# Optimization experiments

Measured on AMD Instinct MI355X. Metric: run time of the kernel, lower is better.

Reference implementation:

```python
import jax, jax.numpy as jnp
import numpy as np

N = 150000
E = 600000
IN_DIM = 128
HID = 64


def setup_inputs() -> dict:
    key = jax.random.key(0)
    ks = jax.random.split(key, 8)
    obs = jax.random.normal(ks[0], (N, IN_DIM), dtype=jnp.float32)
    edge_index = jax.random.randint(ks[1], (2, E), 0, N, dtype=jnp.int64)
    # GCNConv / Linear parameters (PyTorch layout: W is [out, in])
    W1 = jax.random.normal(ks[2], (HID, IN_DIM), dtype=jnp.float32) / np.sqrt(IN_DIM)
    b1 = jnp.zeros((HID,), dtype=jnp.float32)
    W2 = jax.random.normal(ks[3], (HID, HID), dtype=jnp.float32) / np.sqrt(HID)
    b2 = jnp.zeros((HID,), dtype=jnp.float32)
    W3 = jax.random.normal(ks[4], (1, HID), dtype=jnp.float32) / np.sqrt(HID)
    b3 = jnp.zeros((1,), dtype=jnp.float32)
    return {"obs": obs, "edge_index": edge_index, "W1": W1, "b1": b1,
            "W2": W2, "b2": b2, "W3": W3, "b3": b3}


def _gcn_norm(edge_index, n):
    # PyG gcn_norm: add self-loops, symmetric normalization D^-1/2 A D^-1/2
    loops = jnp.arange(n, dtype=edge_index.dtype)
    row = jnp.concatenate([edge_index[0], loops])  # source
    col = jnp.concatenate([edge_index[1], loops])  # target
    deg = jax.ops.segment_sum(jnp.ones(row.shape[0], jnp.float32), col, num_segments=n)
    dinv = jnp.where(deg > 0, jax.lax.rsqrt(deg), 0.0)
    norm = dinv[row] * dinv[col]  # [E+N]
    return row, col, norm


def _gcn_conv(x, row, col, norm, n, W, b):
    # x' = lin(x); out[col] += norm * x'[row]; out += bias
    xw = x @ W.T                     # [N, out]
    msg = xw[row] * norm[:, None]    # gather + scale, [E+N, out]
    out = jax.ops.segment_sum(msg, col, num_segments=n)
    return out + b


def reference(obs, edge_index, W1, b1, W2, b2, W3, b3):
    n = obs.shape[0]
    row, col, norm = _gcn_norm(edge_index, n)
    h1 = jax.nn.relu(_gcn_conv(obs, row, col, norm, n, W1, b1))
    h2 = jax.nn.relu(_gcn_conv(h1, row, col, norm, n, W2, b2))
    out = h2 @ W3.T + b3             # [N, 1]
    out = out.reshape(-1, 15)[:, 3:].reshape(-1)  # drop first 3 of every 15
    return out
```

## Files before the change

kernel.cpp:

```cpp
#include <hip/hip_runtime.h>

#define NN 150000
#define NE 600000
#define IND 128
#define HID 64
#define KMAX 32
#define BSHIFT 9
#define NBUCK 293
#define SUBCAP 384
#define PARTB 586
#define CVTB 32
#define GEMM_GRID ((NN + 63) / 64)
#define NOUT 120000

typedef short s16x8 __attribute__((ext_vector_type(8)));
typedef float f32x4 __attribute__((ext_vector_type(4)));

__device__ __forceinline__ unsigned f2bf(float f) {
    unsigned u = __float_as_uint(f);
    return (u + 0x7FFFu + ((u >> 16) & 1u)) >> 16;
}

#define ACC4(v, dr) \
    a0 = fmaf(__uint_as_float((v).x << 16), dr, a0); \
    a1 = fmaf(__uint_as_float((v).x & 0xFFFF0000u), dr, a1); \
    a2 = fmaf(__uint_as_float((v).y << 16), dr, a2); \
    a3 = fmaf(__uint_as_float((v).y & 0xFFFF0000u), dr, a3);

__global__ void k_zero(int* __restrict__ gcnt) {
    int t = blockIdx.x * 256 + threadIdx.x;
    if (t < NBUCK * 8) gcnt[t] = 0;
}

__global__ __launch_bounds__(256) void k_init(
        const int* __restrict__ rowv, const int* __restrict__ colv,
        int* __restrict__ gcnt, int2* __restrict__ ebuf,
        const float* __restrict__ W1, const float* __restrict__ W2,
        unsigned short* __restrict__ W1b, unsigned short* __restrict__ W2b) {
    int tid = threadIdx.x;
    if (blockIdx.x < PARTB) {
        __shared__ int hist[NBUCK];
        __shared__ int bases[NBUCK];
        for (int i = tid; i < NBUCK; i += 256) hist[i] = 0;
        __syncthreads();
        int t = blockIdx.x * 256 + tid;
        bool valid = (t < NE / 4);
        int4 r4, c4;
        int bk[4], sl[4];
        if (valid) {
            r4 = ((const int4*)rowv)[t];
            c4 = ((const int4*)colv)[t];
            bk[0] = c4.x >> BSHIFT; sl[0] = atomicAdd(&hist[bk[0]], 1);
            bk[1] = c4.y >> BSHIFT; sl[1] = atomicAdd(&hist[bk[1]], 1);
            bk[2] = c4.z >> BSHIFT; sl[2] = atomicAdd(&hist[bk[2]], 1);
            bk[3] = c4.w >> BSHIFT; sl[3] = atomicAdd(&hist[bk[3]], 1);
        }
        __syncthreads();
        int xcd = blockIdx.x & 7;
        for (int i = tid; i < NBUCK; i += 256)
            bases[i] = hist[i] ? atomicAdd(&gcnt[i * 8 + xcd], hist[i]) : 0;
        __syncthreads();
        if (valid) {
            #pragma unroll
            for (int e = 0; e < 4; ++e) {
                int c = (e == 0) ? c4.x : (e == 1) ? c4.y : (e == 2) ? c4.z : c4.w;
                int r = (e == 0) ? r4.x : (e == 1) ? r4.y : (e == 2) ? r4.z : r4.w;
                int p = bases[bk[e]] + sl[e];
                if (p < SUBCAP) ebuf[(bk[e] * 8 + xcd) * SUBCAP + p] = make_int2(c, r);
            }
        }
        return;
    }
    int t = (blockIdx.x - PARTB) * 256 + tid;
    if (t < HID * IND) W1b[t] = (unsigned short)f2bf(W1[t]);
    if (t < HID * HID) W2b[t] = (unsigned short)f2bf(W2[t]);
}

__global__ __launch_bounds__(256) void k_sort_gemm1(
        const float* __restrict__ obs, const unsigned short* __restrict__ W1b,
        unsigned short* __restrict__ xs,
        const int* __restrict__ gcnt, const int2* __restrict__ ebuf,
        int* __restrict__ cursor, float* __restrict__ dinvf,
        int* __restrict__ csr_src) {
    __shared__ char smem[64 * IND * 2];
    int tid = threadIdx.x;
    if (blockIdx.x < NBUCK) {
        int k = blockIdx.x;
        int lo = k << BSHIFT;
        int* cnt = (int*)smem;
        for (int i = tid; i < 512; i += 256) cnt[i] = 0;
        __syncthreads();
        for (int x = 0; x < 8; ++x) {
            int len = gcnt[k * 8 + x]; if (len > SUBCAP) len = SUBCAP;
            const int2* run = ebuf + (size_t)(k * 8 + x) * SUBCAP;
            for (int i = tid; i < len; i += 256) {
                int2 e = run[i];
                int s = atomicAdd(&cnt[e.x - lo], 1);
                if (s < KMAX) csr_src[e.x * KMAX + s] = e.y;
            }
        }
        __syncthreads();
        for (int i = tid; i < 512; i += 256) {
            int n = lo + i;
            if (n < NN) {
                cursor[n] = cnt[i];
                dinvf[n] = rsqrtf((float)(cnt[i] + 1));
            }
        }
        return;
    }
    char* sB = smem;
    int base = (blockIdx.x - NBUCK) * 64;

    {
        const uint4* Wsrc = (const uint4*)W1b;
        for (int idx = tid; idx < 8 * IND; idx += 256) {
            int row = idx >> 4, c8 = idx & 15;
            uint4 v = Wsrc[idx];
            int byte = row * (IND * 2) + c8 * 16;
            byte ^= (row & 7) << 4;
            *(uint4*)(sB + byte) = v;
        }
    }
    __syncthreads();

    int wave = tid >> 6, lane = tid & 63;
    int r16 = lane & 15, kg = lane >> 4;
    int arow = base + 16 * wave + r16;
    if (arow >= NN) arow = NN - 1;
    const float4* Ap = (const float4*)(obs + (size_t)arow * IND) + kg * 2;

    float4 va[8];
    #pragma unroll
    for (int s = 0; s < 4; ++s) {
        va[2 * s]     = Ap[s * 8];
        va[2 * s + 1] = Ap[s * 8 + 1];
    }

    f32x4 acc[4];
    #pragma unroll
    for (int j = 0; j < 4; ++j) acc[j] = (f32x4){0.f, 0.f, 0.f, 0.f};

    #pragma unroll
    for (int s = 0; s < 4; ++s) {
        float4 v0 = va[2 * s], v1 = va[2 * s + 1];
        s16x8 a;
        a[0] = (short)f2bf(v0.x); a[1] = (short)f2bf(v0.y);
        a[2] = (short)f2bf(v0.z); a[3] = (short)f2bf(v0.w);
        a[4] = (short)f2bf(v1.x); a[5] = (short)f2bf(v1.y);
        a[6] = (short)f2bf(v1.z); a[7] = (short)f2bf(v1.w);
        int kb = (s * 32 + kg * 8) * 2;
        #pragma unroll
        for (int j = 0; j < 4; ++j) {
            int row = 16 * j + r16;
            int byte = row * (IND * 2) + kb;
            byte ^= (row & 7) << 4;
            s16x8 b = *(const s16x8*)(sB + byte);
            acc[j] = __builtin_amdgcn_mfma_f32_16x16x32_bf16(a, b, acc[j], 0, 0, 0);
        }
    }

    #pragma unroll
    for (int r = 0; r < 4; ++r) {
        int n = base + 16 * wave + kg * 4 + r;
        if (n >= NN) continue;
        #pragma unroll
        for (int j = 0; j < 4; ++j) {
            int c = 16 * j + r16;
            xs[(size_t)n * HID + c] = (unsigned short)f2bf(acc[j][r]);
        }
    }
}

__global__ __launch_bounds__(256) void k_agg_gemm(
        const unsigned short* __restrict__ xs, const int* __restrict__ cursor,
        const float* __restrict__ dinvf, const int* __restrict__ csr_src,
        const float* __restrict__ bias, const unsigned short* __restrict__ W2b,
        unsigned short* __restrict__ xs2) {
    __shared__ char smem[2 * 64 * HID * 2];
    char* sA = smem;
    char* sB = smem + 64 * HID * 2;
    int tid = threadIdx.x;
    int base = blockIdx.x * 64;

    {
        const uint4* Wsrc = (const uint4*)W2b;
        for (int idx = tid; idx < 8 * HID; idx += 256) {
            int row = idx >> 3, c8 = idx & 7;
            uint4 v = Wsrc[idx];
            int byte = row * (HID * 2) + c8 * 16;
            byte ^= (row & 7) << 4;
            *(uint4*)(sB + byte) = v;
        }
    }

    int lane = tid & 63;
    int l16 = lane & 15, gbase = lane & 48;
    int grp = tid >> 4;
    const uint2* src = (const uint2*)xs;
    float4 bb = ((const float4*)bias)[l16];

    int degA[4], cntA[4], idxA[4];
    uint2 svA[4];
    float drA[4];
    #pragma unroll
    for (int s4 = 0; s4 < 4; ++s4) {
        int node = base + s4 * 16 + grp;
        bool ok = node < NN;
        int nc = ok ? node : NN - 1;
        int deg = cursor[nc];
        degA[s4] = deg;
        cntA[s4] = ok ? (deg < KMAX ? deg : KMAX) : 0;
        idxA[s4] = csr_src[nc * KMAX + l16];
        svA[s4]  = src[(size_t)nc * 16 + l16];
    }
    #pragma unroll
    for (int s4 = 0; s4 < 4; ++s4) {
        int safe = (l16 < cntA[s4]) ? idxA[s4] : 0;
        drA[s4] = dinvf[safe];
    }

    #pragma unroll
    for (int s4 = 0; s4 < 4; ++s4) {
        int row = s4 * 16 + grp;
        int node = base + row;
        int cnt = cntA[s4];
        float dn = rsqrtf((float)(degA[s4] + 1));
        uint2 sv = svA[s4];
        float a0 = __uint_as_float(sv.x << 16) * dn;
        float a1 = __uint_as_float(sv.x & 0xFFFF0000u) * dn;
        float a2 = __uint_as_float(sv.y << 16) * dn;
        float a3 = __uint_as_float(sv.y & 0xFFFF0000u) * dn;
        #pragma unroll
        for (int j = 0; j < 8; ++j) {
            int r    = __shfl(idxA[s4], gbase + j, 64);
            float dr = __shfl(drA[s4], gbase + j, 64);
            if (j < cnt) {
                uint2 v = src[(size_t)r * 16 + l16];
                ACC4(v, dr)
            }
        }
        if (cnt > 8) {
            int c16 = cnt < 16 ? cnt : 16;
            for (int j = 8; j < c16; ++j) {
                int r    = __shfl(idxA[s4], gbase + j, 64);
                float dr = __shfl(drA[s4], gbase + j, 64);
                uint2 v = src[(size_t)r * 16 + l16];
                ACC4(v, dr)
            }
            for (int j = 16; j < cnt; ++j) {
                int r = csr_src[node * KMAX + j];
                float dr = dinvf[r];
                uint2 v = src[(size_t)r * 16 + l16];
                ACC4(v, dr)
            }
        }
        float h0 = fmaxf(fmaf(dn, a0, bb.x), 0.f);
        float h1 = fmaxf(fmaf(dn, a1, bb.y), 0.f);
        float h2 = fmaxf(fmaf(dn, a2, bb.z), 0.f);
        float h3 = fmaxf(fmaf(dn, a3, bb.w), 0.f);
        uint2 o;
        o.x = f2bf(h0) | (f2bf(h1) << 16);
        o.y = f2bf(h2) | (f2bf(h3) << 16);
        if (node >= NN) { o.x = 0u; o.y = 0u; }
        int byte = row * (HID * 2) + l16 * 8;
        byte ^= (row & 7) << 4;
        *(uint2*)(sA + byte) = o;
    }
    __syncthreads();

    int wave = tid >> 6;
    int wr = wave >> 1, wc = wave & 1;
    int r16 = lane & 15, kg = lane >> 4;

    f32x4 acc[2][2];
    #pragma unroll
    for (int i = 0; i < 2; ++i)
        #pragma unroll
        for (int j = 0; j < 2; ++j)
            acc[i][j] = (f32x4){0.f, 0.f, 0.f, 0.f};

    #pragma unroll
    for (int s = 0; s < HID / 32; ++s) {
        int kb = (s * 32 + kg * 8) * 2;
        s16x8 a[2], b[2];
        #pragma unroll
        for (int i = 0; i < 2; ++i) {
            int row = 32 * wr + 16 * i + r16;
            int byte = row * (HID * 2) + kb;
            byte ^= (row & 7) << 4;
            a[i] = *(const s16x8*)(sA + byte);
        }
        #pragma unroll
        for (int j = 0; j < 2; ++j) {
            int row = 32 * wc + 16 * j + r16;
            int byte = row * (HID * 2) + kb;
            byte ^= (row & 7) << 4;
            b[j] = *(const s16x8*)(sB + byte);
        }
        #pragma unroll
        for (int i = 0; i < 2; ++i)
            #pragma unroll
            for (int j = 0; j < 2; ++j)
                acc[i][j] = __builtin_amdgcn_mfma_f32_16x16x32_bf16(a[i], b[j], acc[i][j], 0, 0, 0);
    }

    #pragma unroll
    for (int i = 0; i < 2; ++i) {
        #pragma unroll
        for (int r = 0; r < 4; ++r) {
            int n = base + 32 * wr + 16 * i + kg * 4 + r;
            if (n >= NN) continue;
            float d = dinvf[n];
            #pragma unroll
            for (int j = 0; j < 2; ++j) {
                int c = 32 * wc + 16 * j + r16;
                xs2[(size_t)n * HID + c] = (unsigned short)f2bf(acc[i][j][r] * d);
            }
        }
    }
}

__global__ __launch_bounds__(256) void k_agg_out(const unsigned short* __restrict__ xs,
                      const int* __restrict__ cursor, const int* __restrict__ csr_src,
                      const float* __restrict__ bias, const float* __restrict__ W3,
                      const float* __restrict__ b3, float* __restrict__ outp) {
    int tid = threadIdx.x;
    int lane = tid & 63;
    int l16 = lane & 15, gbase = lane & 48;
    int q = blockIdx.x * 16 + (tid >> 4);
    if (q >= NOUT) return;
    int g15 = q / 12, jj12 = q - g15 * 12;
    int node = g15 * 15 + 3 + jj12;
    int deg = cursor[node];
    int cnt = deg < KMAX ? deg : KMAX;
    float dn = rsqrtf((float)(deg + 1));
    const uint2* src = (const uint2*)xs;
    int idx0 = csr_src[node * KMAX + l16];
    uint2 sv = src[(size_t)node * 16 + l16];
    float a0 = __uint_as_float(sv.x << 16);
    float a1 = __uint_as_float(sv.x & 0xFFFF0000u);
    float a2 = __uint_as_float(sv.y << 16);
    float a3 = __uint_as_float(sv.y & 0xFFFF0000u);
    #pragma unroll
    for (int j = 0; j < 8; ++j) {
        int r = __shfl(idx0, gbase + j, 64);
        if (j < cnt) {
            uint2 v = src[(size_t)r * 16 + l16];
            ACC4(v, 1.0f)
        }
    }
    if (cnt > 8) {
        int c16 = cnt < 16 ? cnt : 16;
        for (int j = 8; j < c16; ++j) {
            int r = __shfl(idx0, gbase + j, 64);
            uint2 v = src[(size_t)r * 16 + l16];
            ACC4(v, 1.0f)
        }
        for (int j = 16; j < cnt; ++j) {
            int r = csr_src[node * KMAX + j];
            uint2 v = src[(size_t)r * 16 + l16];
            ACC4(v, 1.0f)
        }
    }
    float4 bb = ((const float4*)bias)[l16];
    float h0 = fmaxf(fmaf(dn, a0, bb.x), 0.f);
    float h1 = fmaxf(fmaf(dn, a1, bb.y), 0.f);
    float h2 = fmaxf(fmaf(dn, a2, bb.z), 0.f);
    float h3 = fmaxf(fmaf(dn, a3, bb.w), 0.f);
    float4 ww = ((const float4*)W3)[l16];
    float v = h0 * ww.x + h1 * ww.y + h2 * ww.z + h3 * ww.w;
    v += __shfl_xor(v, 1, 64);
    v += __shfl_xor(v, 2, 64);
    v += __shfl_xor(v, 4, 64);
    v += __shfl_xor(v, 8, 64);
    if (l16 == 0) outp[q] = v + b3[0];
}

extern "C" void kernel_launch(void* const* d_in, const int* in_sizes, int n_in,
                              void* d_out, int out_size, void* d_ws, size_t ws_size,
                              hipStream_t stream) {
    const float* obs = (const float*)d_in[0];
    const int*   ei  = (const int*)d_in[1];
    const float* W1  = (const float*)d_in[2];
    const float* b1  = (const float*)d_in[3];
    const float* W2  = (const float*)d_in[4];
    const float* b2  = (const float*)d_in[5];
    const float* W3  = (const float*)d_in[6];
    const float* b3  = (const float*)d_in[7];
    float* out = (float*)d_out;

    char* ws = (char*)d_ws;
    size_t off = 0;
    auto alloc = [&](size_t bytes) -> void* {
        void* p = ws + off;
        off += (bytes + 255) & ~(size_t)255;
        return p;
    };
    int*   gcnt    = (int*)  alloc((size_t)NBUCK * 8 * 4);
    int*   cursor  = (int*)  alloc((size_t)NN * 4);
    float* dinvf   = (float*)alloc((size_t)NN * 4);
    int*   csr_src = (int*)  alloc((size_t)NN * KMAX * 4);
    int2*  ebuf    = (int2*) alloc((size_t)NBUCK * 8 * SUBCAP * 8);
    unsigned short* XB  = (unsigned short*)alloc((size_t)NN * HID * 2);
    unsigned short* XB2 = (unsigned short*)alloc((size_t)NN * HID * 2);
    unsigned short* W1b = (unsigned short*)alloc((size_t)HID * IND * 2);
    unsigned short* W2b = (unsigned short*)alloc((size_t)HID * HID * 2);

    const int* rowv = ei;
    const int* colv = ei + NE;

    k_zero<<<(NBUCK * 8 + 255) / 256, 256, 0, stream>>>(gcnt);
    k_init<<<PARTB + CVTB, 256, 0, stream>>>(rowv, colv, gcnt, ebuf, W1, W2, W1b, W2b);
    k_sort_gemm1<<<NBUCK + GEMM_GRID, 256, 0, stream>>>(obs, W1b, XB, gcnt, ebuf,
                                                        cursor, dinvf, csr_src);
    k_agg_gemm<<<GEMM_GRID, 256, 0, stream>>>(XB, cursor, dinvf, csr_src, b1, W2b, XB2);
    k_agg_out<<<(NOUT + 15) / 16, 256, 0, stream>>>(XB2, cursor, csr_src, b2, W3, b3, out);
}
```

Before: 110.5 us.

## Fuse GEMM1 with edge partitioning, split sort kernel, batch gather loads

GEMM1 (obs×W1) moves into the partition kernel so it runs alongside edge bucketing, and the CSR sort becomes its own kernel with finer 256-node buckets. The weight fp32→bf16 conversion kernel is dropped; each GEMM block converts W1/W2 directly into shared memory. The aggregation loops issue all eight neighbor gathers before accumulating, using zero weights for padding lanes, to raise memory-level parallelism. The cost is redundant per-block weight conversion and extra loads of row 0 for padding lanes. Smaller bucket capacity raises the risk of overflow truncation.

```diff
diff --git a/kernel.cpp b/kernel.cpp
--- a/kernel.cpp
+++ b/kernel.cpp
@@ -5,11 +5,10 @@
 #define IND 128
 #define HID 64
 #define KMAX 32
-#define BSHIFT 9
-#define NBUCK 293
-#define SUBCAP 384
+#define BSHIFT 8
+#define NBUCK 586
+#define SUBCAP 224
 #define PARTB 586
-#define CVTB 32
 #define GEMM_GRID ((NN + 63) / 64)
 #define NOUT 120000
 
@@ -35,12 +34,13 @@
 __global__ __launch_bounds__(256) void k_init(
         const int* __restrict__ rowv, const int* __restrict__ colv,
         int* __restrict__ gcnt, int2* __restrict__ ebuf,
-        const float* __restrict__ W1, const float* __restrict__ W2,
-        unsigned short* __restrict__ W1b, unsigned short* __restrict__ W2b) {
+        const float* __restrict__ obs, const float* __restrict__ W1,
+        unsigned short* __restrict__ xs) {
+    __shared__ char smem[64 * IND * 2];
     int tid = threadIdx.x;
     if (blockIdx.x < PARTB) {
-        __shared__ int hist[NBUCK];
-        __shared__ int bases[NBUCK];
+        int* hist  = (int*)smem;
+        int* bases = hist + NBUCK;
         for (int i = tid; i < NBUCK; i += 256) hist[i] = 0;
         __syncthreads();
         int t = blockIdx.x * 256 + tid;
@@ -71,55 +71,20 @@
         }
         return;
     }
-    int t = (blockIdx.x - PARTB) * 256 + tid;
-    if (t < HID * IND) W1b[t] = (unsigned short)f2bf(W1[t]);
-    if (t < HID * HID) W2b[t] = (unsigned short)f2bf(W2[t]);
-}
-
-__global__ __launch_bounds__(256) void k_sort_gemm1(
-        const float* __restrict__ obs, const unsigned short* __restrict__ W1b,
-        unsigned short* __restrict__ xs,
-        const int* __restrict__ gcnt, const int2* __restrict__ ebuf,
-        int* __restrict__ cursor, float* __restrict__ dinvf,
-        int* __restrict__ csr_src) {
-    __shared__ char smem[64 * IND * 2];
-    int tid = threadIdx.x;
-    if (blockIdx.x < NBUCK) {
-        int k = blockIdx.x;
-        int lo = k << BSHIFT;
-        int* cnt = (int*)smem;
-        for (int i = tid; i < 512; i += 256) cnt[i] = 0;
-        __syncthreads();
-        for (int x = 0; x < 8; ++x) {
-            int len = gcnt[k * 8 + x]; if (len > SUBCAP) len = SUBCAP;
-            const int2* run = ebuf + (size_t)(k * 8 + x) * SUBCAP;
-            for (int i = tid; i < len; i += 256) {
-                int2 e = run[i];
-                int s = atomicAdd(&cnt[e.x - lo], 1);
-                if (s < KMAX) csr_src[e.x * KMAX + s] = e.y;
-            }
-        }
-        __syncthreads();
-        for (int i = tid; i < 512; i += 256) {
-            int n = lo + i;
-            if (n < NN) {
-                cursor[n] = cnt[i];
-                dinvf[n] = rsqrtf((float)(cnt[i] + 1));
-            }
-        }
-        return;
-    }
     char* sB = smem;
-    int base = (blockIdx.x - NBUCK) * 64;
+    int base = (blockIdx.x - PARTB) * 64;
 
     {
-        const uint4* Wsrc = (const uint4*)W1b;
-        for (int idx = tid; idx < 8 * IND; idx += 256) {
-            int row = idx >> 4, c8 = idx & 15;
-            uint4 v = Wsrc[idx];
-            int byte = row * (IND * 2) + c8 * 16;
+        const float4* Wsrc = (const float4*)W1;
+        for (int idx = tid; idx < 64 * 32; idx += 256) {
+            int row = idx >> 5, c4i = idx & 31;
+            float4 w = Wsrc[idx];
+            uint2 p;
+            p.x = f2bf(w.x) | (f2bf(w.y) << 16);
+            p.y = f2bf(w.z) | (f2bf(w.w) << 16);
+            int byte = row * (IND * 2) + c4i * 8;
             byte ^= (row & 7) << 4;
-            *(uint4*)(sB + byte) = v;
+            *(uint2*)(sB + byte) = p;
         }
     }
     __syncthreads();
@@ -172,10 +137,37 @@
     }
 }
 
+__global__ __launch_bounds__(256) void k_sort(
+        const int* __restrict__ gcnt, const int2* __restrict__ ebuf,
+        int* __restrict__ cursor, float* __restrict__ dinvf,
+        int* __restrict__ csr_src) {
+    __shared__ int cnt[256];
+    int tid = threadIdx.x;
+    int k = blockIdx.x;
+    int lo = k << BSHIFT;
+    cnt[tid] = 0;
+    __syncthreads();
+    for (int x = 0; x < 8; ++x) {
+        int len = gcnt[k * 8 + x]; if (len > SUBCAP) len = SUBCAP;
+        const int2* run = ebuf + (size_t)(k * 8 + x) * SUBCAP;
+        for (int i = tid; i < len; i += 256) {
+            int2 e = run[i];
+            int s = atomicAdd(&cnt[e.x - lo], 1);
+            if (s < KMAX) csr_src[e.x * KMAX + s] = e.y;
+        }
+    }
+    __syncthreads();
+    int n = lo + tid;
+    if (n < NN) {
+        cursor[n] = cnt[tid];
+        dinvf[n] = rsqrtf((float)(cnt[tid] + 1));
+    }
+}
+
 __global__ __launch_bounds__(256) void k_agg_gemm(
         const unsigned short* __restrict__ xs, const int* __restrict__ cursor,
         const float* __restrict__ dinvf, const int* __restrict__ csr_src,
-        const float* __restrict__ bias, const unsigned short* __restrict__ W2b,
+        const float* __restrict__ bias, const float* __restrict__ W2,
         unsigned short* __restrict__ xs2) {
     __shared__ char smem[2 * 64 * HID * 2];
     char* sA = smem;
@@ -184,13 +176,16 @@
     int base = blockIdx.x * 64;
 
     {
-        const uint4* Wsrc = (const uint4*)W2b;
-        for (int idx = tid; idx < 8 * HID; idx += 256) {
-            int row = idx >> 3, c8 = idx & 7;
-            uint4 v = Wsrc[idx];
-            int byte = row * (HID * 2) + c8 * 16;
+        const float4* Wsrc = (const float4*)W2;
+        for (int idx = tid; idx < 64 * 16; idx += 256) {
+            int row = idx >> 4, c4i = idx & 15;
+            float4 w = Wsrc[idx];
+            uint2 p;
+            p.x = f2bf(w.x) | (f2bf(w.y) << 16);
+            p.y = f2bf(w.z) | (f2bf(w.w) << 16);
+            int byte = row * (HID * 2) + c4i * 8;
             byte ^= (row & 7) << 4;
-            *(uint4*)(sB + byte) = v;
+            *(uint2*)(sB + byte) = p;
         }
     }
 
@@ -216,8 +211,7 @@
     }
     #pragma unroll
     for (int s4 = 0; s4 < 4; ++s4) {
-        int safe = (l16 < cntA[s4]) ? idxA[s4] : 0;
-        drA[s4] = dinvf[safe];
+        drA[s4] = (l16 < cntA[s4]) ? dinvf[idxA[s4]] : 0.0f;
     }
 
     #pragma unroll
@@ -231,28 +225,31 @@
         float a1 = __uint_as_float(sv.x & 0xFFFF0000u) * dn;
         float a2 = __uint_as_float(sv.y << 16) * dn;
         float a3 = __uint_as_float(sv.y & 0xFFFF0000u) * dn;
+        uint2 v[8];
         #pragma unroll
         for (int j = 0; j < 8; ++j) {
-            int r    = __shfl(idxA[s4], gbase + j, 64);
+            int r = __shfl(idxA[s4], gbase + j, 64);
+            r = (j < cnt) ? r : 0;
+            v[j] = src[(size_t)r * 16 + l16];
+        }
+        #pragma unroll
+        for (int j = 0; j < 8; ++j) {
             float dr = __shfl(drA[s4], gbase + j, 64);
-            if (j < cnt) {
-                uint2 v = src[(size_t)r * 16 + l16];
-                ACC4(v, dr)
-            }
+            ACC4(v[j], dr)
         }
         if (cnt > 8) {
             int c16 = cnt < 16 ? cnt : 16;
             for (int j = 8; j < c16; ++j) {
                 int r    = __shfl(idxA[s4], gbase + j, 64);
                 float dr = __shfl(drA[s4], gbase + j, 64);
-                uint2 v = src[(size_t)r * 16 + l16];
-                ACC4(v, dr)
+                uint2 vv = src[(size_t)r * 16 + l16];
+                ACC4(vv, dr)
             }
             for (int j = 16; j < cnt; ++j) {
                 int r = csr_src[node * KMAX + j];
                 float dr = dinvf[r];
-                uint2 v = src[(size_t)r * 16 + l16];
-                ACC4(v, dr)
+                uint2 vv = src[(size_t)r * 16 + l16];
+                ACC4(vv, dr)
             }
         }
         float h0 = fmaxf(fmaf(dn, a0, bb.x), 0.f);
@@ -337,30 +334,35 @@
     float dn = rsqrtf((float)(deg + 1));
     const uint2* src = (const uint2*)xs;
     int idx0 = csr_src[node * KMAX + l16];
+    float w0 = (l16 < cnt) ? 1.0f : 0.0f;
     uint2 sv = src[(size_t)node * 16 + l16];
     float a0 = __uint_as_float(sv.x << 16);
     float a1 = __uint_as_float(sv.x & 0xFFFF0000u);
     float a2 = __uint_as_float(sv.y << 16);
     float a3 = __uint_as_float(sv.y & 0xFFFF0000u);
+    uint2 v[8];
     #pragma unroll
     for (int j = 0; j < 8; ++j) {
         int r = __shfl(idx0, gbase + j, 64);
-        if (j < cnt) {
-            uint2 v = src[(size_t)r * 16 + l16];
-            ACC4(v, 1.0f)
-        }
+        r = (j < cnt) ? r : 0;
+        v[j] = src[(size_t)r * 16 + l16];
+    }
+    #pragma unroll
+    for (int j = 0; j < 8; ++j) {
+        float w = __shfl(w0, gbase + j, 64);
+        ACC4(v[j], w)
     }
     if (cnt > 8) {
         int c16 = cnt < 16 ? cnt : 16;
         for (int j = 8; j < c16; ++j) {
             int r = __shfl(idx0, gbase + j, 64);
-            uint2 v = src[(size_t)r * 16 + l16];
-            ACC4(v, 1.0f)
+            uint2 vv = src[(size_t)r * 16 + l16];
+            ACC4(vv, 1.0f)
         }
         for (int j = 16; j < cnt; ++j) {
             int r = csr_src[node * KMAX + j];
-            uint2 v = src[(size_t)r * 16 + l16];
-            ACC4(v, 1.0f)
+            uint2 vv = src[(size_t)r * 16 + l16];
+            ACC4(vv, 1.0f)
         }
     }
     float4 bb = ((const float4*)bias)[l16];
@@ -369,12 +371,12 @@
     float h2 = fmaxf(fmaf(dn, a2, bb.z), 0.f);
     float h3 = fmaxf(fmaf(dn, a3, bb.w), 0.f);
     float4 ww = ((const float4*)W3)[l16];
-    float v = h0 * ww.x + h1 * ww.y + h2 * ww.z + h3 * ww.w;
-    v += __shfl_xor(v, 1, 64);
-    v += __shfl_xor(v, 2, 64);
-    v += __shfl_xor(v, 4, 64);
-    v += __shfl_xor(v, 8, 64);
-    if (l16 == 0) outp[q] = v + b3[0];
+    float v3 = h0 * ww.x + h1 * ww.y + h2 * ww.z + h3 * ww.w;
+    v3 += __shfl_xor(v3, 1, 64);
+    v3 += __shfl_xor(v3, 2, 64);
+    v3 += __shfl_xor(v3, 4, 64);
+    v3 += __shfl_xor(v3, 8, 64);
+    if (l16 == 0) outp[q] = v3 + b3[0];
 }
 
 extern "C" void kernel_launch(void* const* d_in, const int* in_sizes, int n_in,
@@ -404,16 +406,13 @@
     int2*  ebuf    = (int2*) alloc((size_t)NBUCK * 8 * SUBCAP * 8);
     unsigned short* XB  = (unsigned short*)alloc((size_t)NN * HID * 2);
     unsigned short* XB2 = (unsigned short*)alloc((size_t)NN * HID * 2);
-    unsigned short* W1b = (unsigned short*)alloc((size_t)HID * IND * 2);
-    unsigned short* W2b = (unsigned short*)alloc((size_t)HID * HID * 2);
 
     const int* rowv = ei;
     const int* colv = ei + NE;
 
     k_zero<<<(NBUCK * 8 + 255) / 256, 256, 0, stream>>>(gcnt);
-    k_init<<<PARTB + CVTB, 256, 0, stream>>>(rowv, colv, gcnt, ebuf, W1, W2, W1b, W2b);
-    k_sort_gemm1<<<NBUCK + GEMM_GRID, 256, 0, stream>>>(obs, W1b, XB, gcnt, ebuf,
-                                                        cursor, dinvf, csr_src);
-    k_agg_gemm<<<GEMM_GRID, 256, 0, stream>>>(XB, cursor, dinvf, csr_src, b1, W2b, XB2);
+    k_init<<<PARTB + GEMM_GRID, 256, 0, stream>>>(rowv, colv, gcnt, ebuf, obs, W1, XB);
+    k_sort<<<NBUCK, 256, 0, stream>>>(gcnt, ebuf, cursor, dinvf, csr_src);
+    k_agg_gemm<<<GEMM_GRID, 256, 0, stream>>>(XB, cursor, dinvf, csr_src, b1, W2, XB2);
     k_agg_out<<<(NOUT + 15) / 16, 256, 0, stream>>>(XB2, cursor, csr_src, b2, W3, b3, out);
 }
```

After: 107.8 us. -2.5%, faster.
